# Kernel tuning notes

Measured on AMD Instinct MI355X. Metric: run time of the kernel, lower is better.

## Reference

```python
import jax, jax.numpy as jnp
import numpy as np

B, S, Db, E, T = 64, 512, 768, 50, 68
NC, NT, K, V = 16, 8, 3, 100
MAXLEN = 8


def _make_spans(k1, k2, n):
    starts = jax.random.randint(k1, (B, n), 0, S - MAXLEN)
    lens = jax.random.randint(k2, (B, n), 1, MAXLEN + 1)
    return jnp.stack([starts, starts + lens], axis=-1)  # [B,n,2] half-open


def setup_inputs() -> dict:
    key = jax.random.key(0)
    ks = jax.random.split(key, 12)
    enc = jax.random.normal(ks[0], (B, S, Db), jnp.float32)
    entity_table = jax.random.normal(ks[1], (V, E), jnp.float32) * 0.02
    entity_table = entity_table.at[0].set(0.0)  # padding_idx=0
    fc1_w = jax.random.normal(ks[2], (Db, Db + E), jnp.float32) * 0.02
    fc1_b = jnp.zeros((Db,), jnp.float32)
    trig_w = jax.random.normal(ks[3], (T, Db), jnp.float32) * 0.02
    trig_b = jnp.zeros((T,), jnp.float32)
    entities_x = jax.random.randint(ks[4], (B, S, K), 0, V)
    head_idx = jax.random.randint(ks[5], (B, S), 0, S)
    cand_spans = _make_spans(ks[6], ks[7], NC)
    trig_spans = _make_spans(ks[8], ks[9], NT)
    return {"enc": enc, "entity_table": entity_table, "fc1_w": fc1_w,
            "fc1_b": fc1_b, "trig_w": trig_w, "trig_b": trig_b,
            "entities_x": entities_x, "head_idx": head_idx,
            "cand_spans": cand_spans, "trig_spans": trig_spans}


def _span_mean(x, spans):
    # x: [B,S,D], spans: [B,N,2] half-open -> [B,N,D] mean over span tokens
    pos = jnp.arange(x.shape[1])
    mask = (pos[None, None, :] >= spans[..., 0:1]) & (pos[None, None, :] < spans[..., 1:2])
    m = mask.astype(x.dtype)  # [B,N,S]
    cnt = jnp.maximum(m.sum(-1, keepdims=True), 1.0)
    return jnp.einsum('bns,bsd->bnd', m, x) / cnt


def reference(enc, entity_table, fc1_w, fc1_b, trig_w, trig_b,
              entities_x, head_idx, cand_spans, trig_spans):
    # multi-label entity embedding: sum over K label slots (padding row is zero)
    ent = entity_table[entities_x].sum(axis=2)            # [B,S,E]
    x = jnp.concatenate([enc, ent], axis=-1)              # [B,S,Db+E]
    x = jax.nn.relu(jnp.einsum('bsd,hd->bsh', x, fc1_w) + fc1_b)  # fc1 (dropout=eval)
    # per-sample index_select over sequence dim (wordpiece head gather)
    x = jnp.take_along_axis(x, head_idx[:, :, None], axis=1)      # [B,S,768]
    trigger_logits = jnp.einsum('bsh,th->bst', x, trig_w) + trig_b  # [B,S,T]
    trigger_hat = jnp.argmax(trigger_logits, axis=-1)
    # span mean-pooling for predicted triggers and golden entity candidates
    ev = _span_mean(x, trig_spans)                        # [B,NT,768]
    en = _span_mean(x, cand_spans)                        # [B,NC,768]
    ev_e = jnp.broadcast_to(ev[:, :, None, :], (B, NT, NC, Db))
    en_e = jnp.broadcast_to(en[:, None, :, :], (B, NT, NC, Db))
    argument_hidden = jnp.concatenate([ev_e, en_e], axis=-1)  # [B,NT,NC,1536]
    return trigger_logits, trigger_hat, argument_hidden
```

## Files before the change

### kernel.cpp

```cpp
#include <hip/hip_runtime.h>

#define BS_TOTAL 32768
#define DB 768
#define KV 832
#define KREAL 818
#define TT 68
#define SEQ 512

typedef float v2f __attribute__((ext_vector_type(2)));
typedef float f32x4 __attribute__((ext_vector_type(4)));
typedef _Float16 f16x8 __attribute__((ext_vector_type(8)));
typedef _Float16 f16x4 __attribute__((ext_vector_type(4)));
typedef unsigned int uint;
typedef unsigned short ushort;

union U4 { uint4 u; f16x8 h; };

__device__ __forceinline__ _Float16 us2h(ushort x){ union{ushort u;_Float16 h;}c; c.u=x; return c.h; }
__device__ __forceinline__ ushort h2us(_Float16 x){ union{ushort u;_Float16 h;}c; c.h=x; return c.u; }
__device__ __forceinline__ uint packx(float xs){
    _Float16 h=(_Float16)xs; _Float16 l=(_Float16)(xs-(float)h);
    return (uint)h2us(h) | ((uint)h2us(l)<<16);
}

__global__ __launch_bounds__(64) void packwf_kernel(
    const float* __restrict__ W, _Float16* __restrict__ Wf)
{
    const int bid = blockIdx.x;
    const int l = threadIdx.x;
    const int bn = bid / 208;
    const int rem = bid % 208;
    const int kt = rem >> 4;
    const int sub = rem & 15;
    const int ks = sub >> 3;
    const int nfg = sub & 7;
    const int row = bn * 128 + nfg * 16 + (l & 15);
    const int kb = kt * 64 + ks * 32 + ((l >> 4) << 3);
    f16x8 hi, lo;
#pragma unroll
    for (int q = 0; q < 8; ++q) {
        int k = kb + q;
        float v = (k < KREAL) ? W[(size_t)row * KREAL + k] * 1024.f : 0.f;
        _Float16 h = (_Float16)v;
        hi[q] = h; lo[q] = (_Float16)(v - (float)h);
    }
    const size_t fb = ((((size_t)bn * 13 + kt) * 2 + ks) * 8 + nfg) * 2;
    *reinterpret_cast<f16x8*>(Wf + (fb + 0) * 512 + l * 8) = hi;
    *reinterpret_cast<f16x8*>(Wf + (fb + 1) * 512 + l * 8) = lo;
}

__global__ __launch_bounds__(256) void splitw_trig(
    const float* __restrict__ Wt, _Float16* __restrict__ T0, _Float16* __restrict__ T1)
{
    int r2 = blockIdx.x;
    int t = threadIdx.x;
#pragma unroll
    for (int j = 0; j < 3; ++j) {
        int k = t * 3 + j;
        if (k < DB) {
            float v = (r2 < TT) ? Wt[(size_t)r2 * DB + k] * 1024.f : 0.f;
            _Float16 h = (_Float16)v;
            T0[(size_t)r2 * DB + k] = h;
            T1[(size_t)r2 * DB + k] = (_Float16)(v - (float)h);
        }
    }
}

__global__ __launch_bounds__(256, 2) void fc1_mfma(
    const float* __restrict__ enc, const int* __restrict__ ex,
    const float* __restrict__ table, const _Float16* __restrict__ Wf,
    const float* __restrict__ bias, uint* __restrict__ xout)
{
    __shared__ char lds[32768];
    char* sA0 = lds;
    char* sA1 = lds + 16384;
    const int t = threadIdx.x;
    const int l = t & 63;
    const int w = t >> 6;
    const int wr = w >> 1, wc = w & 1;
    const int lr = l & 15, hi2 = l >> 4;
    const int bm0 = blockIdx.x * 128;
    const int by = blockIdx.y;
    const int bn0 = by * 128;

    f32x4 acc[4][4];
#pragma unroll
    for (int i = 0; i < 4; ++i)
#pragma unroll
        for (int j = 0; j < 4; ++j) acc[i][j] = (f32x4){0.f, 0.f, 0.f, 0.f};

    float4 pa[8];
    uint4 bf[8];

    auto loadA = [&](int k0) {
        if (k0 < DB) {
#pragma unroll
            for (int c = 0; c < 8; ++c) {
                int idx = t + c * 256;
                int r = idx >> 4;
                int c4 = (idx & 15) << 2;
                pa[c] = *reinterpret_cast<const float4*>(enc + (size_t)(bm0 + r) * DB + k0 + c4);
            }
        } else {
#pragma unroll
            for (int c = 0; c < 8; ++c) {
                int idx = t + c * 256;
                int r = idx >> 4;
                int c4 = (idx & 15) << 2;
                const int* exr = ex + (size_t)(bm0 + r) * 3;
                int i0 = exr[0] * 50, i1 = exr[1] * 50, i2 = exr[2] * 50;
                float vv[4];
#pragma unroll
                for (int j = 0; j < 4; ++j) {
                    int e = c4 + j;
                    vv[j] = (e < 50) ? (table[i0 + e] + table[i1 + e] + table[i2 + e]) : 0.f;
                }
                pa[c] = make_float4(vv[0], vv[1], vv[2], vv[3]);
            }
        }
    };
    auto loadBf = [&](int kt, int ks) {
        const size_t fb = ((((size_t)by * 13 + kt) * 2 + ks) * 8 + wc * 4) * 2;
        const _Float16* base = Wf + fb * 512 + l * 8;
#pragma unroll
        for (int q = 0; q < 8; ++q)
            bf[q] = *reinterpret_cast<const uint4*>(base + (size_t)q * 512);
    };

    loadA(0); loadBf(0, 0);

    for (int kt = 0; kt < 13; ++kt) {
        __syncthreads();
#pragma unroll
        for (int c = 0; c < 8; ++c) {
            int idx = t + c * 256;
            int r = idx >> 4;
            int b0 = (idx & 15) << 3;
            int off = (r << 7) + (b0 ^ ((r & 7) << 4));
            float f0 = pa[c].x * 32.f, f1 = pa[c].y * 32.f;
            float f2 = pa[c].z * 32.f, f3 = pa[c].w * 32.f;
            _Float16 h0 = (_Float16)f0, h1 = (_Float16)f1, h2 = (_Float16)f2, h3 = (_Float16)f3;
            f16x4 hi = {h0, h1, h2, h3};
            f16x4 lo = {(_Float16)(f0 - (float)h0), (_Float16)(f1 - (float)h1),
                        (_Float16)(f2 - (float)h2), (_Float16)(f3 - (float)h3)};
            *reinterpret_cast<f16x4*>(sA0 + off) = hi;
            *reinterpret_cast<f16x4*>(sA1 + off) = lo;
        }
        __syncthreads();
        if (kt < 12) loadA((kt + 1) * 64);
#pragma unroll
        for (int ks = 0; ks < 2; ++ks) {
            const int kb = ks * 64 + (hi2 << 4);
            f16x8 a0f[4], a1f[4], b0f[4], b1f[4];
#pragma unroll
            for (int mf = 0; mf < 4; ++mf) {
                int r = wr * 64 + mf * 16 + lr;
                int off = (r << 7) + (kb ^ ((r & 7) << 4));
                a0f[mf] = *reinterpret_cast<const f16x8*>(sA0 + off);
                a1f[mf] = *reinterpret_cast<const f16x8*>(sA1 + off);
            }
#pragma unroll
            for (int nf = 0; nf < 4; ++nf) {
                U4 u0, u1;
                u0.u = bf[nf * 2 + 0];
                u1.u = bf[nf * 2 + 1];
                b0f[nf] = u0.h;
                b1f[nf] = u1.h;
            }
            if (ks == 0) loadBf(kt, 1);
            else if (kt < 12) loadBf(kt + 1, 0);
#pragma unroll
            for (int mf = 0; mf < 4; ++mf)
#pragma unroll
                for (int nf = 0; nf < 4; ++nf) {
                    acc[mf][nf] = __builtin_amdgcn_mfma_f32_16x16x32_f16(a0f[mf], b0f[nf], acc[mf][nf], 0, 0, 0);
                    acc[mf][nf] = __builtin_amdgcn_mfma_f32_16x16x32_f16(a1f[mf], b0f[nf], acc[mf][nf], 0, 0, 0);
                    acc[mf][nf] = __builtin_amdgcn_mfma_f32_16x16x32_f16(a0f[mf], b1f[nf], acc[mf][nf], 0, 0, 0);
                }
        }
    }

    const float inv0 = 1.0f / 32768.f;
    uint* sE = reinterpret_cast<uint*>(lds);
    float bv[4];
#pragma unroll
    for (int nf = 0; nf < 4; ++nf) bv[nf] = bias[bn0 + wc * 64 + nf * 16 + lr];

#pragma unroll
    for (int p = 0; p < 4; ++p) {
        __syncthreads();
        if (wr == (p >> 1)) {
#pragma unroll
            for (int mi = 0; mi < 2; ++mi) {
                int mf = (p & 1) * 2 + mi;
                int rowl = mf * 16 + hi2 * 4 - (p & 1) * 32;
#pragma unroll
                for (int nf = 0; nf < 4; ++nf) {
                    int col = wc * 64 + nf * 16 + lr;
#pragma unroll
                    for (int j = 0; j < 4; ++j) {
                        float x = fmaxf(acc[mf][nf][j] * inv0 + bv[nf], 0.f);
                        sE[(rowl + j) * 132 + col] = packx(x * 256.f);
                    }
                }
            }
        }
        __syncthreads();
        int rrow = t >> 3;
        int c0 = (t & 7) << 4;
        uint* gp = xout + (size_t)(bm0 + p * 32 + rrow) * DB + bn0 + c0;
        const uint* sp = sE + rrow * 132 + c0;
#pragma unroll
        for (int q = 0; q < 4; ++q)
            *reinterpret_cast<uint4*>(gp + q * 4) = *reinterpret_cast<const uint4*>(sp + q * 4);
    }
}

__global__ __launch_bounds__(256, 4) void trig_mfma(
    const uint* __restrict__ xfc, const int* __restrict__ head_idx,
    const _Float16* __restrict__ T0, const _Float16* __restrict__ T1,
    const float* __restrict__ bt, float* __restrict__ logits, float* __restrict__ hat)
{
    __shared__ char sA[16384];
    __shared__ char sW[20480];
    __shared__ int srow[64];
    const int t = threadIdx.x;
    const int l = t & 63;
    const int w = t >> 6;
    const int lr = l & 15, hi2 = l >> 4;
    const int s0 = blockIdx.x * 64;
    if (t < 64) srow[t] = (((s0 + t) >> 9) << 9) + head_idx[s0 + t];
    __syncthreads();

    f32x4 acc[5];
#pragma unroll
    for (int n = 0; n < 5; ++n) acc[n] = (f32x4){0.f, 0.f, 0.f, 0.f};

    uint4 pa[4];
    uint4 pw[5];

    auto loadA = [&](int k0) {
        int r = t >> 2, c16 = (t & 3) << 4;
        const uint* src = xfc + (size_t)srow[r] * DB + k0 + c16;
#pragma unroll
        for (int q = 0; q < 4; ++q) pa[q] = *reinterpret_cast<const uint4*>(src + q * 4);
    };
    auto loadW = [&](int k0) {
#pragma unroll
        for (int i = 0; i < 5; ++i) {
            int cid = t + i * 256;
            int row = cid >> 4;
            int sl = cid & 15;
            const _Float16* src = ((sl >> 3) ? T1 : T0) + (size_t)row * DB + k0 + (sl & 7) * 8;
            pw[i] = *reinterpret_cast<const uint4*>(src);
        }
    };

    loadA(0); loadW(0);

    for (int kt = 0; kt < 12; ++kt) {
        __syncthreads();
        {
            int r = t >> 2, c16 = (t & 3) << 4;
            int sw = (r & 7) << 4;
            uint uu[16];
#pragma unroll
            for (int q = 0; q < 4; ++q) *reinterpret_cast<uint4*>(uu + q * 4) = pa[q];
            U4 h0, h1, l0, l1;
#pragma unroll
            for (int j = 0; j < 8; ++j) {
                h0.h[j] = us2h((ushort)(uu[j] & 0xffff));
                l0.h[j] = us2h((ushort)(uu[j] >> 16));
                h1.h[j] = us2h((ushort)(uu[8 + j] & 0xffff));
                l1.h[j] = us2h((ushort)(uu[8 + j] >> 16));
            }
            int bh = c16 * 2;
            *reinterpret_cast<uint4*>(sA + (r << 8) + ((bh +  0) ^ sw)) = h0.u;
            *reinterpret_cast<uint4*>(sA + (r << 8) + ((bh + 16) ^ sw)) = h1.u;
            *reinterpret_cast<uint4*>(sA + (r << 8) + (128 + ((bh +  0) ^ sw))) = l0.u;
            *reinterpret_cast<uint4*>(sA + (r << 8) + (128 + ((bh + 16) ^ sw))) = l1.u;
        }
#pragma unroll
        for (int i = 0; i < 5; ++i) {
            int cid = t + i * 256;
            int row = cid >> 4;
            int sl = cid & 15;
            int sw = (row & 7) << 4;
            int byte = (sl >> 3) * 128 + (((sl & 7) * 16) ^ sw);
            *reinterpret_cast<uint4*>(sW + (row << 8) + byte) = pw[i];
        }
        __syncthreads();
        if (kt < 11) { loadA((kt + 1) * 64); loadW((kt + 1) * 64); }
#pragma unroll
        for (int ks = 0; ks < 2; ++ks) {
            int hb = ks * 64 + hi2 * 16;
            int rA = w * 16 + lr;
            int swA = (rA & 7) << 4;
            f16x8 ah = *reinterpret_cast<const f16x8*>(sA + (rA << 8) + (hb ^ swA));
            f16x8 al = *reinterpret_cast<const f16x8*>(sA + (rA << 8) + (128 + (hb ^ swA)));
#pragma unroll
            for (int nf = 0; nf < 5; ++nf) {
                int rB = nf * 16 + lr;
                int swB = (rB & 7) << 4;
                f16x8 bh = *reinterpret_cast<const f16x8*>(sW + (rB << 8) + (hb ^ swB));
                f16x8 bl = *reinterpret_cast<const f16x8*>(sW + (rB << 8) + (128 + (hb ^ swB)));
                acc[nf] = __builtin_amdgcn_mfma_f32_16x16x32_f16(ah, bh, acc[nf], 0, 0, 0);
                acc[nf] = __builtin_amdgcn_mfma_f32_16x16x32_f16(al, bh, acc[nf], 0, 0, 0);
                acc[nf] = __builtin_amdgcn_mfma_f32_16x16x32_f16(ah, bl, acc[nf], 0, 0, 0);
            }
        }
    }

    const float inv = 1.0f / 262144.f;
#pragma unroll
    for (int j = 0; j < 4; ++j) {
        int row = s0 + w * 16 + hi2 * 4 + j;
        float bestv = -1e38f;
        int besti = 0;
#pragma unroll
        for (int nf = 0; nf < 5; ++nf) {
            int col = nf * 16 + lr;
            float v = -1e38f;
            if (col < TT) {
                v = acc[nf][j] * inv + bt[col];
                logits[(size_t)row * TT + col] = v;
            }
            if (v > bestv) { bestv = v; besti = col; }
        }
#pragma unroll
        for (int off = 8; off > 0; off >>= 1) {
            float ov = __shfl_xor(bestv, off, 16);
            int oi = __shfl_xor(besti, off, 16);
            if (ov > bestv || (ov == bestv && oi < besti)) { bestv = ov; besti = oi; }
        }
        if (lr == 0) hat[row] = (float)besti;
    }
}

__global__ __launch_bounds__(256) void pool_kernel(
    const uint* __restrict__ xfc, const int* __restrict__ head_idx,
    const int* __restrict__ cand_spans, const int* __restrict__ trig_spans,
    float* __restrict__ pooled)
{
    const int n = blockIdx.x;
    const int b = blockIdx.y;
    __shared__ int sh_rows[8];
    __shared__ int sh_len;
    __shared__ int sh_st;
    __shared__ float sh_inv;
    const int t = threadIdx.x;
    if (t == 0) {
        const int* sp = (n < 8) ? (trig_spans + (b * 8 + n) * 2)
                                : (cand_spans + (b * 16 + (n - 8)) * 2);
        int st = sp[0], en = sp[1];
        int len = en - st;
        if (len < 0) len = 0;
        if (len > 8) len = 8;
        sh_len = len;
        sh_st = st;
        sh_inv = (1.f / (float)(len > 0 ? len : 1)) * (1.f / 256.f);
    }
    __syncthreads();
    if (t < sh_len) sh_rows[t] = (b << 9) + head_idx[(b << 9) + sh_st + t];
    __syncthreads();
    const int len = sh_len;
    const float inv = sh_inv;
#pragma unroll
    for (int j = 0; j < 3; ++j) {
        int c = t + j * 256;
        float s = 0.f;
        for (int p = 0; p < len; ++p) {
            uint u = xfc[(size_t)sh_rows[p] * DB + c];
            s += (float)us2h((ushort)(u & 0xffff)) + (float)us2h((ushort)(u >> 16));
        }
        pooled[((size_t)b * 24 + n) * DB + c] = s * inv;
    }
}

__global__ __launch_bounds__(256) void arg_kernel(
    const float* __restrict__ pooled, float* __restrict__ out2)
{
    int g = blockIdx.x * 256 + threadIdx.x;
    int b = g / 49152;
    int rem = g - b * 49152;
    int pair = rem / 384;
    int off4 = rem - pair * 384;
    int ti = pair >> 4;
    int c = pair & 15;
    int col = off4 << 2;
    const float* src;
    if (col < DB) src = pooled + ((size_t)(b * 24 + ti)) * DB + col;
    else          src = pooled + ((size_t)(b * 24 + 8 + c)) * DB + (col - DB);
    float4 v = *reinterpret_cast<const float4*>(src);
    *reinterpret_cast<float4*>(out2 + ((size_t)g << 2)) = v;
}

extern "C" void kernel_launch(void* const* d_in, const int* in_sizes, int n_in,
                              void* d_out, int out_size, void* d_ws, size_t ws_size,
                              hipStream_t stream)
{
    const float* enc   = (const float*)d_in[0];
    const float* table = (const float*)d_in[1];
    const float* fc1w  = (const float*)d_in[2];
    const float* fc1b  = (const float*)d_in[3];
    const float* trigw = (const float*)d_in[4];
    const float* trigb = (const float*)d_in[5];
    const int*   ex    = (const int*)d_in[6];
    const int*   hidx  = (const int*)d_in[7];
    const int*   cspan = (const int*)d_in[8];
    const int*   tspan = (const int*)d_in[9];

    float* out0 = (float*)d_out;
    float* out1 = out0 + (size_t)BS_TOTAL * TT;
    float* out2 = out1 + BS_TOTAL;

    uint*  ws_xfc  = (uint*)d_ws;
    float* ws_pool = (float*)(ws_xfc + (size_t)BS_TOTAL * DB);
    _Float16* wsWf = (_Float16*)(ws_pool + (size_t)64 * 24 * DB);
    _Float16* wsT0 = wsWf + (size_t)2496 * 512;
    _Float16* wsT1 = wsT0 + (size_t)80 * DB;

    packwf_kernel<<<dim3(1248), dim3(64), 0, stream>>>(fc1w, wsWf);
    splitw_trig<<<dim3(80), dim3(256), 0, stream>>>(trigw, wsT0, wsT1);
    fc1_mfma<<<dim3(BS_TOTAL / 128, DB / 128), dim3(256), 0, stream>>>(
        enc, ex, table, wsWf, fc1b, ws_xfc);
    trig_mfma<<<dim3(BS_TOTAL / 64), dim3(256), 0, stream>>>(
        ws_xfc, hidx, wsT0, wsT1, trigb, out0, out1);
    pool_kernel<<<dim3(24, 64), dim3(256), 0, stream>>>(ws_xfc, hidx, cspan, tspan, ws_pool);
    arg_kernel<<<dim3(3145728 / 256), dim3(256), 0, stream>>>(ws_pool, out2);
}
```

Baseline: 250.4 us.

## Presplit fc1 activations into fp16 hi/lo buffers and remap block order

```diff
diff --git a/kernel.cpp b/kernel.cpp
--- a/kernel.cpp
+++ b/kernel.cpp
@@ -21,6 +21,40 @@
 __device__ __forceinline__ uint packx(float xs){
     _Float16 h=(_Float16)xs; _Float16 l=(_Float16)(xs-(float)h);
     return (uint)h2us(h) | ((uint)h2us(l)<<16);
+}
+
+__global__ __launch_bounds__(256) void presplit_kernel(
+    const float* __restrict__ enc, const int* __restrict__ ex,
+    const float* __restrict__ table,
+    _Float16* __restrict__ Ahi, _Float16* __restrict__ Alo)
+{
+    int g = blockIdx.x * 256 + threadIdx.x;
+    int row = g / 104;
+    int c8 = (g - row * 104) * 8;
+    float v[8];
+    if (c8 < DB) {
+        float4 f0 = *reinterpret_cast<const float4*>(enc + (size_t)row * DB + c8);
+        float4 f1 = *reinterpret_cast<const float4*>(enc + (size_t)row * DB + c8 + 4);
+        v[0]=f0.x; v[1]=f0.y; v[2]=f0.z; v[3]=f0.w;
+        v[4]=f1.x; v[5]=f1.y; v[6]=f1.z; v[7]=f1.w;
+    } else {
+        const int* exr = ex + (size_t)row * 3;
+        int i0 = exr[0] * 50, i1 = exr[1] * 50, i2 = exr[2] * 50;
+#pragma unroll
+        for (int j = 0; j < 8; ++j) {
+            int e = c8 + j - DB;
+            v[j] = (e < 50) ? (table[i0 + e] + table[i1 + e] + table[i2 + e]) : 0.f;
+        }
+    }
+    f16x8 hi, lo;
+#pragma unroll
+    for (int j = 0; j < 8; ++j) {
+        float s = v[j] * 32.f;
+        _Float16 h = (_Float16)s;
+        hi[j] = h; lo[j] = (_Float16)(s - (float)h);
+    }
+    *reinterpret_cast<f16x8*>(Ahi + (size_t)row * KV + c8) = hi;
+    *reinterpret_cast<f16x8*>(Alo + (size_t)row * KV + c8) = lo;
 }
 
 __global__ __launch_bounds__(64) void packwf_kernel(
@@ -67,8 +101,8 @@
 }
 
 __global__ __launch_bounds__(256, 2) void fc1_mfma(
-    const float* __restrict__ enc, const int* __restrict__ ex,
-    const float* __restrict__ table, const _Float16* __restrict__ Wf,
+    const _Float16* __restrict__ Ahi, const _Float16* __restrict__ Alo,
+    const _Float16* __restrict__ Wf,
     const float* __restrict__ bias, uint* __restrict__ xout)
 {
     __shared__ char lds[32768];
@@ -79,8 +113,10 @@
     const int w = t >> 6;
     const int wr = w >> 1, wc = w & 1;
     const int lr = l & 15, hi2 = l >> 4;
-    const int bm0 = blockIdx.x * 128;
-    const int by = blockIdx.y;
+    const int bid = blockIdx.x;
+    const int wgid = (bid & 7) * 192 + (bid >> 3);
+    const int bm0 = (wgid / 6) * 128;
+    const int by = wgid % 6;
     const int bn0 = by * 128;
 
     f32x4 acc[4][4];
@@ -89,34 +125,19 @@
 #pragma unroll
         for (int j = 0; j < 4; ++j) acc[i][j] = (f32x4){0.f, 0.f, 0.f, 0.f};
 
-    float4 pa[8];
+    uint4 pa[8];
     uint4 bf[8];
 
-    auto loadA = [&](int k0) {
-        if (k0 < DB) {
-#pragma unroll
-            for (int c = 0; c < 8; ++c) {
-                int idx = t + c * 256;
-                int r = idx >> 4;
-                int c4 = (idx & 15) << 2;
-                pa[c] = *reinterpret_cast<const float4*>(enc + (size_t)(bm0 + r) * DB + k0 + c4);
-            }
-        } else {
-#pragma unroll
-            for (int c = 0; c < 8; ++c) {
-                int idx = t + c * 256;
-                int r = idx >> 4;
-                int c4 = (idx & 15) << 2;
-                const int* exr = ex + (size_t)(bm0 + r) * 3;
-                int i0 = exr[0] * 50, i1 = exr[1] * 50, i2 = exr[2] * 50;
-                float vv[4];
-#pragma unroll
-                for (int j = 0; j < 4; ++j) {
-                    int e = c4 + j;
-                    vv[j] = (e < 50) ? (table[i0 + e] + table[i1 + e] + table[i2 + e]) : 0.f;
-                }
-                pa[c] = make_float4(vv[0], vv[1], vv[2], vv[3]);
-            }
+    auto loadA = [&](int kt) {
+        const int k0 = kt * 64;
+#pragma unroll
+        for (int c = 0; c < 4; ++c) {
+            int idx = t + c * 256;
+            int r = idx >> 3;
+            int h8 = (idx & 7) << 3;
+            size_t goff = (size_t)(bm0 + r) * KV + k0 + h8;
+            pa[c]     = *reinterpret_cast<const uint4*>(Ahi + goff);
+            pa[c + 4] = *reinterpret_cast<const uint4*>(Alo + goff);
         }
     };
     auto loadBf = [&](int kt, int ks) {
@@ -132,22 +153,16 @@
     for (int kt = 0; kt < 13; ++kt) {
         __syncthreads();
 #pragma unroll
-        for (int c = 0; c < 8; ++c) {
+        for (int c = 0; c < 4; ++c) {
             int idx = t + c * 256;
-            int r = idx >> 4;
-            int b0 = (idx & 15) << 3;
-            int off = (r << 7) + (b0 ^ ((r & 7) << 4));
-            float f0 = pa[c].x * 32.f, f1 = pa[c].y * 32.f;
-            float f2 = pa[c].z * 32.f, f3 = pa[c].w * 32.f;
-            _Float16 h0 = (_Float16)f0, h1 = (_Float16)f1, h2 = (_Float16)f2, h3 = (_Float16)f3;
-            f16x4 hi = {h0, h1, h2, h3};
-            f16x4 lo = {(_Float16)(f0 - (float)h0), (_Float16)(f1 - (float)h1),
-                        (_Float16)(f2 - (float)h2), (_Float16)(f3 - (float)h3)};
-            *reinterpret_cast<f16x4*>(sA0 + off) = hi;
-            *reinterpret_cast<f16x4*>(sA1 + off) = lo;
-        }
-        __syncthreads();
-        if (kt < 12) loadA((kt + 1) * 64);
+            int r = idx >> 3;
+            int b16 = (idx & 7) << 4;
+            int off = (r << 7) + (b16 ^ ((r & 7) << 4));
+            *reinterpret_cast<uint4*>(sA0 + off) = pa[c];
+            *reinterpret_cast<uint4*>(sA1 + off) = pa[c + 4];
+        }
+        __syncthreads();
+        if (kt < 12) loadA(kt + 1);
 #pragma unroll
         for (int ks = 0; ks < 2; ++ks) {
             const int kb = ks * 64 + (hi2 << 4);
@@ -416,14 +431,16 @@
 
     uint*  ws_xfc  = (uint*)d_ws;
     float* ws_pool = (float*)(ws_xfc + (size_t)BS_TOTAL * DB);
-    _Float16* wsWf = (_Float16*)(ws_pool + (size_t)64 * 24 * DB);
-    _Float16* wsT0 = wsWf + (size_t)2496 * 512;
-    _Float16* wsT1 = wsT0 + (size_t)80 * DB;
-
+    _Float16* wsWf  = (_Float16*)(ws_pool + (size_t)64 * 24 * DB);
+    _Float16* wsT0  = wsWf + (size_t)2496 * 512;
+    _Float16* wsT1  = wsT0 + (size_t)80 * DB;
+    _Float16* wsAhi = wsT1 + (size_t)80 * DB;
+    _Float16* wsAlo = wsAhi + (size_t)BS_TOTAL * KV;
+
+    presplit_kernel<<<dim3(BS_TOTAL * 104 / 256), dim3(256), 0, stream>>>(enc, ex, table, wsAhi, wsAlo);
     packwf_kernel<<<dim3(1248), dim3(64), 0, stream>>>(fc1w, wsWf);
     splitw_trig<<<dim3(80), dim3(256), 0, stream>>>(trigw, wsT0, wsT1);
-    fc1_mfma<<<dim3(BS_TOTAL / 128, DB / 128), dim3(256), 0, stream>>>(
-        enc, ex, table, wsWf, fc1b, ws_xfc);
+    fc1_mfma<<<dim3(1536), dim3(256), 0, stream>>>(wsAhi, wsAlo, wsWf, fc1b, ws_xfc);
     trig_mfma<<<dim3(BS_TOTAL / 64), dim3(256), 0, stream>>>(
         ws_xfc, hidx, wsT0, wsT1, trigb, out0, out1);
     pool_kernel<<<dim3(24, 64), dim3(256), 0, stream>>>(ws_xfc, hidx, cspan, tspan, ws_pool);
```

Result: slower. 391.9 us (+56.5%).
